# Kernel optimization log

Measured on AMD Instinct MI355X. Metric: run time of the kernel, lower is better.

Reference implementation:

```python
import jax, jax.numpy as jnp
import numpy as np

N, E = 50000, 800000
IN_DIM, HIDDEN, OUT_DIM, LAYERS = 128, 64, 40, 3


def setup_inputs() -> dict:
    key = jax.random.key(0)
    ks = jax.random.split(key, 12)
    glorot = lambda k, fi, fo: jax.random.normal(k, (fi, fo), jnp.float32) * np.sqrt(2.0 / (fi + fo)).astype(np.float32)
    return {
        "x": jax.random.normal(ks[0], (N, IN_DIM), jnp.float32),
        "edge_index": jax.random.randint(ks[1], (2, E), 0, N, jnp.int64),
        "edge_weight": jax.random.uniform(ks[2], (E,), jnp.float32),
        "W1": glorot(ks[3], IN_DIM, HIDDEN), "b1": jnp.zeros((HIDDEN,), jnp.float32),
        "W2": glorot(ks[4], HIDDEN, HIDDEN), "b2": jnp.zeros((HIDDEN,), jnp.float32),
        "W3": glorot(ks[5], HIDDEN, HIDDEN), "b3": jnp.zeros((HIDDEN,), jnp.float32),
        "Wlin": glorot(ks[6], HIDDEN * LAYERS, OUT_DIM), "blin": jnp.zeros((OUT_DIM,), jnp.float32),
    }


def reference(x, edge_index, edge_weight, W1, b1, W2, b2, W3, b3, Wlin, blin):
    src, dst = edge_index[0], edge_index[1]

    def gcn_conv(h, W, b):
        # GCNConv with normalize=False: linear transform, then weighted sum aggregation at dst, then bias.
        h = h @ W                                   # [N, hidden]
        msg = h[src] * edge_weight[:, None]          # [E, hidden] gather + scale
        agg = jax.ops.segment_sum(msg, dst, num_segments=h.shape[0])  # scatter-add
        return agg + b

    outs = []
    h = x
    for W, b in ((W1, b1), (W2, b2), (W3, b3)):
        h = jax.nn.relu(gcn_conv(h, W, b))           # dropout is identity at inference
        outs.append(h)

    hjk = jnp.concatenate(outs, axis=-1)             # JumpingKnowledge mode='cat' -> [N, hidden*layers]
    return hjk @ Wlin + blin                         # [N, out_dim]
```

## Files before the change

### kernel.cpp

```cpp
#include <hip/hip_runtime.h>

#define HID 64
#define JK_DIM 192
#define OUT_DIM 40
#define AP 136
#define HP 72
#define W_PITCH 196
#define FG_PITCH 44

typedef __attribute__((ext_vector_type(8))) short bf16x8;
typedef __attribute__((ext_vector_type(4))) float f32x4;

__device__ inline unsigned short f2b(float f) {
    unsigned u = __float_as_uint(f);
    unsigned r = u + 0x7FFF + ((u >> 16) & 1);
    return (unsigned short)(r >> 16);
}
__device__ inline float b2f(unsigned short u) {
    return __uint_as_float(((unsigned)u) << 16);
}
__device__ inline float blo(unsigned u) { return __uint_as_float(u << 16); }
__device__ inline float bhi(unsigned u) { return __uint_as_float(u & 0xFFFF0000u); }
__device__ inline unsigned pack2(float a, float b) {
    return (unsigned)f2b(a) | ((unsigned)f2b(b) << 16);
}

__global__ __launch_bounds__(256) void prep(int* __restrict__ deg, int n,
                                            const float* __restrict__ W,
                                            float* __restrict__ Wt,
                                            int* __restrict__ gctr) {
    int i = blockIdx.x * 256 + threadIdx.x;
    if (i == 0) gctr[0] = 0;
    if (i < n) deg[i] = 0;
    if (i < JK_DIM * OUT_DIM) {
        int k = i / OUT_DIM;
        int c = i - k * OUT_DIM;
        Wt[c * JK_DIM + k] = W[i];
    }
}

__global__ __launch_bounds__(256) void hist_dst(const int* __restrict__ dst,
                                                int* __restrict__ deg,
                                                unsigned short* __restrict__ rank,
                                                int E, int part) {
    int p = blockIdx.x & 7;
    int bid = blockIdx.x >> 3;
    int nblk = gridDim.x >> 3;
    int lo = p * part, hi = lo + part;
    int E4 = E >> 2;
    for (int q = bid * 256 + threadIdx.x; q < E4; q += nblk * 256) {
        int4 d4 = ((const int4*)dst)[q];
        int e = q * 4;
        if (d4.x >= lo && d4.x < hi) rank[e + 0] = (unsigned short)atomicAdd(&deg[d4.x], 1);
        if (d4.y >= lo && d4.y < hi) rank[e + 1] = (unsigned short)atomicAdd(&deg[d4.y], 1);
        if (d4.z >= lo && d4.z < hi) rank[e + 2] = (unsigned short)atomicAdd(&deg[d4.z], 1);
        if (d4.w >= lo && d4.w < hi) rank[e + 3] = (unsigned short)atomicAdd(&deg[d4.w], 1);
    }
    if (bid == 0 && threadIdx.x < (E & 3)) {
        int e = (E & ~3) + threadIdx.x;
        int d = dst[e];
        if (d >= lo && d < hi) rank[e] = (unsigned short)atomicAdd(&deg[d], 1);
    }
}

__global__ __launch_bounds__(256) void scan_fused(const int* __restrict__ deg,
                                                  int* __restrict__ off,
                                                  int* __restrict__ gctr, int n) {
    __shared__ int tmp[256];
    __shared__ int base;
    int i = blockIdx.x * 256 + threadIdx.x;
    int v = (i < n) ? deg[i] : 0;
    tmp[threadIdx.x] = v;
    __syncthreads();
    for (int d = 1; d < 256; d <<= 1) {
        int t = (threadIdx.x >= d) ? tmp[threadIdx.x - d] : 0;
        __syncthreads();
        tmp[threadIdx.x] += t;
        __syncthreads();
    }
    if (threadIdx.x == 255) base = atomicAdd(gctr, tmp[255]);
    __syncthreads();
    if (i < n) off[i] = base + tmp[threadIdx.x] - v;
}

__global__ __launch_bounds__(256) void fill_and_gemm(
        const int* __restrict__ src, const int* __restrict__ dst,
        const float* __restrict__ ew, const int* __restrict__ off,
        const unsigned short* __restrict__ rank,
        unsigned* __restrict__ ecsr, int E,
        const float* __restrict__ x, const float* __restrict__ W1,
        unsigned short* __restrict__ linb, int n, int nFill) {
    __shared__ unsigned short Ah[64 * AP];
    __shared__ unsigned short Wt[64 * AP];
    int tid = threadIdx.x;
    if ((int)blockIdx.x < nFill) {
        int q = blockIdx.x * 256 + tid;
        int E4 = E >> 2;
        if (q < E4) {
            int4 d4 = ((const int4*)dst)[q];
            int4 s4 = ((const int4*)src)[q];
            float4 wv = ((const float4*)ew)[q];
            ushort4 r4 = ((const ushort4*)rank)[q];
            ecsr[off[d4.x] + r4.x] = (unsigned)s4.x | ((unsigned)f2b(wv.x) << 16);
            ecsr[off[d4.y] + r4.y] = (unsigned)s4.y | ((unsigned)f2b(wv.y) << 16);
            ecsr[off[d4.z] + r4.z] = (unsigned)s4.z | ((unsigned)f2b(wv.z) << 16);
            ecsr[off[d4.w] + r4.w] = (unsigned)s4.w | ((unsigned)f2b(wv.w) << 16);
        }
        if (blockIdx.x == 0 && tid < (E & 3)) {
            int e = (E & ~3) + tid;
            int d = dst[e];
            ecsr[off[d] + rank[e]] = (unsigned)src[e] | ((unsigned)f2b(ew[e]) << 16);
        }
        return;
    }
    int row0 = (blockIdx.x - nFill) * 64;
    if (row0 >= n) return;
    for (int i = tid; i < 64 * 32; i += 256) {
        int r = i >> 5;
        int c4 = (i & 31) * 4;
        int grow = row0 + r;
        if (grow >= n) grow = n - 1;
        float4 v = *(const float4*)(x + (long)grow * 128 + c4);
        ushort4 o;
        o.x = f2b(v.x); o.y = f2b(v.y); o.z = f2b(v.z); o.w = f2b(v.w);
        *(ushort4*)(Ah + r * AP + c4) = o;
    }
    for (int i = tid; i < 128 * 16; i += 256) {
        int k = i >> 4;
        int n4 = (i & 15) * 4;
        float4 v = *(const float4*)(W1 + (long)k * 64 + n4);
        Wt[(n4 + 0) * AP + k] = f2b(v.x);
        Wt[(n4 + 1) * AP + k] = f2b(v.y);
        Wt[(n4 + 2) * AP + k] = f2b(v.z);
        Wt[(n4 + 3) * AP + k] = f2b(v.w);
    }
    __syncthreads();

    int wave = tid >> 6;
    int lane = tid & 63;
    int lr = lane & 15;
    int lk = (lane >> 4) * 8;
    f32x4 acc[4];
#pragma unroll
    for (int nf = 0; nf < 4; ++nf) acc[nf] = (f32x4){0.f, 0.f, 0.f, 0.f};
#pragma unroll
    for (int k0 = 0; k0 < 128; k0 += 32) {
        bf16x8 a = *(const bf16x8*)(Ah + (wave * 16 + lr) * AP + k0 + lk);
#pragma unroll
        for (int nf = 0; nf < 4; ++nf) {
            bf16x8 b = *(const bf16x8*)(Wt + (nf * 16 + lr) * AP + k0 + lk);
            acc[nf] = __builtin_amdgcn_mfma_f32_16x16x32_bf16(a, b, acc[nf], 0, 0, 0);
        }
    }
    int mbase = wave * 16 + (lane >> 4) * 4;
#pragma unroll
    for (int nf = 0; nf < 4; ++nf) {
#pragma unroll
        for (int r = 0; r < 4; ++r) {
            int grow = row0 + mbase + r;
            if (grow < n)
                linb[(long)grow * HID + nf * 16 + lr] = f2b(acc[nf][r]);
        }
    }
}

__global__ __launch_bounds__(256) void aggregate(const unsigned short* __restrict__ linb,
                                                 const unsigned* __restrict__ ecsr,
                                                 const int* __restrict__ off,
                                                 const int* __restrict__ deg,
                                                 const float* __restrict__ bias,
                                                 unsigned short* __restrict__ hout, int n) {
    int cl = threadIdx.x & 7;
    float4 bLo = *(const float4*)(bias + cl * 8);
    float4 bHi = *(const float4*)(bias + cl * 8 + 4);
    int grp = (blockIdx.x * 256 + threadIdx.x) >> 3;
    int ngrp = (gridDim.x * 256) >> 3;
    for (int node = grp; node < n; node += ngrp) {
        int start = off[node];
        int cnt = deg[node];
        float acc[8];
#pragma unroll
        for (int i = 0; i < 8; ++i) acc[i] = 0.f;

        int s[8];
        float w[8];
#pragma unroll
        for (int t = 0; t < 8; ++t) {
            s[t] = 0; w[t] = 0.f;
            if (t < cnt) {
                unsigned m = ecsr[start + t];
                s[t] = (int)(m & 0xFFFFu);
                w[t] = b2f((unsigned short)(m >> 16));
            }
        }
        for (int bb = 0; bb < cnt; bb += 8) {
            int s2[8];
            float w2[8];
#pragma unroll
            for (int t = 0; t < 8; ++t) {
                int e = bb + 8 + t;
                s2[t] = 0; w2[t] = 0.f;
                if (e < cnt) {
                    unsigned m = ecsr[start + e];
                    s2[t] = (int)(m & 0xFFFFu);
                    w2[t] = b2f((unsigned short)(m >> 16));
                }
            }
            uint4 u[8];
#pragma unroll
            for (int t = 0; t < 8; ++t)
                u[t] = *(const uint4*)(linb + (long)s[t] * HID + cl * 8);
#pragma unroll
            for (int t = 0; t < 8; ++t) {
                acc[0] += blo(u[t].x) * w[t];
                acc[1] += bhi(u[t].x) * w[t];
                acc[2] += blo(u[t].y) * w[t];
                acc[3] += bhi(u[t].y) * w[t];
                acc[4] += blo(u[t].z) * w[t];
                acc[5] += bhi(u[t].z) * w[t];
                acc[6] += blo(u[t].w) * w[t];
                acc[7] += bhi(u[t].w) * w[t];
            }
#pragma unroll
            for (int t = 0; t < 8; ++t) { s[t] = s2[t]; w[t] = w2[t]; }
        }

        uint4 o;
        o.x = pack2(fmaxf(acc[0] + bLo.x, 0.f), fmaxf(acc[1] + bLo.y, 0.f));
        o.y = pack2(fmaxf(acc[2] + bLo.z, 0.f), fmaxf(acc[3] + bLo.w, 0.f));
        o.z = pack2(fmaxf(acc[4] + bHi.x, 0.f), fmaxf(acc[5] + bHi.y, 0.f));
        o.w = pack2(fmaxf(acc[6] + bHi.z, 0.f), fmaxf(acc[7] + bHi.w, 0.f));
        *(uint4*)(hout + (long)node * JK_DIM + cl * 8) = o;
    }
}

__global__ __launch_bounds__(256) void agg_transform(
        const unsigned short* __restrict__ hprev,
        const unsigned* __restrict__ ecsr,
        const int* __restrict__ off, const int* __restrict__ deg,
        const float* __restrict__ W, const float* __restrict__ bias,
        unsigned short* __restrict__ hout, int n) {
    __shared__ unsigned short Hs[64 * HP];
    __shared__ unsigned short Wt[64 * HP];
    int tid = threadIdx.x;
    int row0 = blockIdx.x * 64;
    if (row0 >= n) return;
    for (int i = tid; i < 64 * 16; i += 256) {
        int k = i >> 4;
        int n4 = (i & 15) * 4;
        float4 v = *(const float4*)(W + (long)k * 64 + n4);
        Wt[(n4 + 0) * HP + k] = f2b(v.x);
        Wt[(n4 + 1) * HP + k] = f2b(v.y);
        Wt[(n4 + 2) * HP + k] = f2b(v.z);
        Wt[(n4 + 3) * HP + k] = f2b(v.w);
    }
    int cl = tid & 7;
    int g0 = tid >> 3;
    for (int gi = 0; gi < 2; ++gi) {
        int lrow = g0 + gi * 32;
        int node = row0 + lrow;
        float acc[8];
#pragma unroll
        for (int i = 0; i < 8; ++i) acc[i] = 0.f;
        if (node < n) {
            int start = off[node];
            int cnt = deg[node];
            int s[8];
            float w[8];
#pragma unroll
            for (int t = 0; t < 8; ++t) {
                s[t] = 0; w[t] = 0.f;
                if (t < cnt) {
                    unsigned m = ecsr[start + t];
                    s[t] = (int)(m & 0xFFFFu);
                    w[t] = b2f((unsigned short)(m >> 16));
                }
            }
            for (int bb = 0; bb < cnt; bb += 8) {
                int s2[8];
                float w2[8];
#pragma unroll
                for (int t = 0; t < 8; ++t) {
                    int e = bb + 8 + t;
                    s2[t] = 0; w2[t] = 0.f;
                    if (e < cnt) {
                        unsigned m = ecsr[start + e];
                        s2[t] = (int)(m & 0xFFFFu);
                        w2[t] = b2f((unsigned short)(m >> 16));
                    }
                }
                uint4 u[8];
#pragma unroll
                for (int t = 0; t < 8; ++t)
                    u[t] = *(const uint4*)(hprev + (long)s[t] * JK_DIM + cl * 8);
#pragma unroll
                for (int t = 0; t < 8; ++t) {
                    acc[0] += blo(u[t].x) * w[t];
                    acc[1] += bhi(u[t].x) * w[t];
                    acc[2] += blo(u[t].y) * w[t];
                    acc[3] += bhi(u[t].y) * w[t];
                    acc[4] += blo(u[t].z) * w[t];
                    acc[5] += bhi(u[t].z) * w[t];
                    acc[6] += blo(u[t].w) * w[t];
                    acc[7] += bhi(u[t].w) * w[t];
                }
#pragma unroll
                for (int t = 0; t < 8; ++t) { s[t] = s2[t]; w[t] = w2[t]; }
            }
        }
        uint4 o;
        o.x = pack2(acc[0], acc[1]);
        o.y = pack2(acc[2], acc[3]);
        o.z = pack2(acc[4], acc[5]);
        o.w = pack2(acc[6], acc[7]);
        *(uint4*)(Hs + lrow * HP + cl * 8) = o;
    }
    __syncthreads();
    int wave = tid >> 6;
    int lane = tid & 63;
    int lr = lane & 15;
    int lk = (lane >> 4) * 8;
    f32x4 d[4];
#pragma unroll
    for (int nf = 0; nf < 4; ++nf) d[nf] = (f32x4){0.f, 0.f, 0.f, 0.f};
#pragma unroll
    for (int k0 = 0; k0 < 64; k0 += 32) {
        bf16x8 a = *(const bf16x8*)(Hs + (wave * 16 + lr) * HP + k0 + lk);
#pragma unroll
        for (int nf = 0; nf < 4; ++nf) {
            bf16x8 b = *(const bf16x8*)(Wt + (nf * 16 + lr) * HP + k0 + lk);
            d[nf] = __builtin_amdgcn_mfma_f32_16x16x32_bf16(a, b, d[nf], 0, 0, 0);
        }
    }
    int mbase = wave * 16 + (lane >> 4) * 4;
#pragma unroll
    for (int nf = 0; nf < 4; ++nf) {
        float bv = bias[nf * 16 + lr];
#pragma unroll
        for (int r = 0; r < 4; ++r) {
            int grow = row0 + mbase + r;
            if (grow < n)
                hout[(long)grow * JK_DIM + nf * 16 + lr] = f2b(fmaxf(d[nf][r] + bv, 0.f));
        }
    }
}

__global__ __launch_bounds__(256) void final_gemm(const unsigned short* __restrict__ hcat,
                                                  const float* __restrict__ Wt,
                                                  const float* __restrict__ b,
                                                  float* __restrict__ out, int n) {
    __shared__ float pool[OUT_DIM * W_PITCH];
    int tid = threadIdx.x;
    for (int i = tid; i < OUT_DIM * 48; i += 256) {
        int c = i / 48;
        int q = (i - c * 48) * 4;
        *(float4*)(pool + c * W_PITCH + q) = *(const float4*)(Wt + (long)c * JK_DIM + q);
    }
    __syncthreads();

    int rg = tid >> 3;
    int cg = tid & 7;
    int c0 = cg * 5;
    int row0 = blockIdx.x * 64;
    int r0 = row0 + rg * 2;
    int ra = r0 < n ? r0 : n - 1;
    int rb = r0 + 1 < n ? r0 + 1 : n - 1;
    const unsigned short* ha = hcat + (long)ra * JK_DIM;
    const unsigned short* hb = hcat + (long)rb * JK_DIM;

    float acc[2][5];
#pragma unroll
    for (int r = 0; r < 2; ++r)
#pragma unroll
        for (int i = 0; i < 5; ++i) acc[r][i] = 0.f;

#pragma unroll 4
    for (int k = 0; k < JK_DIM; k += 4) {
        uint2 ua = *(const uint2*)(ha + k);
        uint2 ub = *(const uint2*)(hb + k);
        float4 va = make_float4(blo(ua.x), bhi(ua.x), blo(ua.y), bhi(ua.y));
        float4 vb = make_float4(blo(ub.x), bhi(ub.x), blo(ub.y), bhi(ub.y));
        float4 w0 = *(const float4*)(pool + (c0 + 0) * W_PITCH + k);
        float4 w1 = *(const float4*)(pool + (c0 + 1) * W_PITCH + k);
        float4 w2 = *(const float4*)(pool + (c0 + 2) * W_PITCH + k);
        float4 w3 = *(const float4*)(pool + (c0 + 3) * W_PITCH + k);
        float4 w4 = *(const float4*)(pool + (c0 + 4) * W_PITCH + k);
        acc[0][0] += va.x * w0.x + va.y * w0.y + va.z * w0.z + va.w * w0.w;
        acc[0][1] += va.x * w1.x + va.y * w1.y + va.z * w1.z + va.w * w1.w;
        acc[0][2] += va.x * w2.x + va.y * w2.y + va.z * w2.z + va.w * w2.w;
        acc[0][3] += va.x * w3.x + va.y * w3.y + va.z * w3.z + va.w * w3.w;
        acc[0][4] += va.x * w4.x + va.y * w4.y + va.z * w4.z + va.w * w4.w;
        acc[1][0] += vb.x * w0.x + vb.y * w0.y + vb.z * w0.z + vb.w * w0.w;
        acc[1][1] += vb.x * w1.x + vb.y * w1.y + vb.z * w1.z + vb.w * w1.w;
        acc[1][2] += vb.x * w2.x + vb.y * w2.y + vb.z * w2.z + vb.w * w2.w;
        acc[1][3] += vb.x * w3.x + vb.y * w3.y + vb.z * w3.z + vb.w * w3.w;
        acc[1][4] += vb.x * w4.x + vb.y * w4.y + vb.z * w4.z + vb.w * w4.w;
    }

    __syncthreads();
#pragma unroll
    for (int r = 0; r < 2; ++r)
#pragma unroll
        for (int i = 0; i < 5; ++i)
            pool[(rg * 2 + r) * FG_PITCH + c0 + i] = acc[r][i] + b[c0 + i];
    __syncthreads();

    if (row0 + 64 <= n) {
        for (int i = tid; i < 64 * OUT_DIM / 4; i += 256) {
            int f = i * 4;
            int row = f / OUT_DIM;
            int col = f - row * OUT_DIM;
            *(float4*)(out + (long)(row0 + row) * OUT_DIM + col) =
                *(const float4*)(pool + row * FG_PITCH + col);
        }
    } else {
        for (int i = tid; i < 64 * OUT_DIM; i += 256) {
            int row = i / OUT_DIM;
            int col = i - row * OUT_DIM;
            if (row0 + row < n)
                out[(long)(row0 + row) * OUT_DIM + col] = pool[row * FG_PITCH + col];
        }
    }
}

extern "C" void kernel_launch(void* const* d_in, const int* in_sizes, int n_in,
                              void* d_out, int out_size, void* d_ws, size_t ws_size,
                              hipStream_t stream) {
    const float* x    = (const float*)d_in[0];
    const int*   ei   = (const int*)d_in[1];
    const float* ew   = (const float*)d_in[2];
    const float* W1   = (const float*)d_in[3];
    const float* b1   = (const float*)d_in[4];
    const float* W2   = (const float*)d_in[5];
    const float* b2   = (const float*)d_in[6];
    const float* W3   = (const float*)d_in[7];
    const float* b3   = (const float*)d_in[8];
    const float* Wlin = (const float*)d_in[9];
    const float* blin = (const float*)d_in[10];
    float* out = (float*)d_out;

    const int N = in_sizes[0] / 128;
    const int E = in_sizes[2];
    const int* src = ei;
    const int* dst = ei + E;
    const int PART = (N + 7) / 8;

    char* wsb = (char*)d_ws;
    unsigned short* linb  = (unsigned short*)wsb;   wsb += (long)N * HID * 2;
    unsigned short* hcatb = (unsigned short*)wsb;   wsb += (long)N * JK_DIM * 2;
    int* deg    = (int*)wsb;                        wsb += (long)N * 4;
    int* off    = (int*)wsb;                        wsb += (long)N * 4;
    int* bsum   = (int*)wsb;                        wsb += 256 * 4;
    float* Wt   = (float*)wsb;                      wsb += (long)JK_DIM * OUT_DIM * 4;
    unsigned* ecsr = (unsigned*)wsb;
    unsigned short* rank = hcatb;
    int* gctr = bsum;

    dim3 blk(256);
    const int nblkN = (N + 255) / 256;
    dim3 gN(nblkN);
    dim3 gHist(8 * 104);
    const int nFill = ((E >> 2) + 255) / 256;
    const int nGemm = (N + 63) / 64;
    dim3 gFG(nFill + nGemm);
    dim3 gTile((N + 63) / 64);
    dim3 gAgg((N + 31) / 32);
    dim3 gFin((N + 63) / 64);

    unsigned short* h1 = hcatb;
    unsigned short* h2 = hcatb + HID;
    unsigned short* h3 = hcatb + 2 * HID;

    prep<<<gN, blk, 0, stream>>>(deg, N, Wlin, Wt, gctr);
    hist_dst<<<gHist, blk, 0, stream>>>(dst, deg, rank, E, PART);
    scan_fused<<<gN, blk, 0, stream>>>(deg, off, gctr, N);

    fill_and_gemm<<<gFG, blk, 0, stream>>>(src, dst, ew, off, rank, ecsr, E,
                                           x, W1, linb, N, nFill);
    aggregate<<<gAgg, blk, 0, stream>>>(linb, ecsr, off, deg, b1, h1, N);

    agg_transform<<<gTile, blk, 0, stream>>>(h1, ecsr, off, deg, W2, b2, h2, N);
    agg_transform<<<gTile, blk, 0, stream>>>(h2, ecsr, off, deg, W3, b3, h3, N);

    final_gemm<<<gFin, blk, 0, stream>>>(hcatb, Wt, blin, out, N);
}
```

Measured before the change: 257.5 us.

## Fuse final JK linear into last agg_transform and balance rows via atomic counter

Removes the separate final_gemm kernel by computing the JumpingKnowledge output projection inside the third-layer agg_transform. The layer-3 activations stay in shared memory instead of being written to and re-read from global memory, and the Wlin weights are read from global/L1 rather than staged in LDS. It also replaces the fixed two-rows-per-group split of the aggregation loop with a shared atomic row counter, so groups of 8 lanes pull rows dynamically to even out uneven degree work. The fused tail does more per-thread scalar FMAs with uncoalesced weight loads and raises register pressure.

```diff
diff --git a/kernel.cpp b/kernel.cpp
--- a/kernel.cpp
+++ b/kernel.cpp
@@ -5,8 +5,6 @@
 #define OUT_DIM 40
 #define AP 136
 #define HP 72
-#define W_PITCH 196
-#define FG_PITCH 44
 
 typedef __attribute__((ext_vector_type(8))) short bf16x8;
 typedef __attribute__((ext_vector_type(4))) float f32x4;
@@ -239,12 +237,18 @@
         const unsigned* __restrict__ ecsr,
         const int* __restrict__ off, const int* __restrict__ deg,
         const float* __restrict__ W, const float* __restrict__ bias,
-        unsigned short* __restrict__ hout, int n) {
+        unsigned short* __restrict__ hout, int n,
+        const unsigned short* __restrict__ hcat,
+        const float* __restrict__ WtLin,
+        const float* __restrict__ blin,
+        float* __restrict__ outp) {
     __shared__ unsigned short Hs[64 * HP];
     __shared__ unsigned short Wt[64 * HP];
+    __shared__ int nextRow;
     int tid = threadIdx.x;
     int row0 = blockIdx.x * 64;
     if (row0 >= n) return;
+    if (tid == 0) nextRow = 0;
     for (int i = tid; i < 64 * 16; i += 256) {
         int k = i >> 4;
         int n4 = (i & 15) * 4;
@@ -254,10 +258,14 @@
         Wt[(n4 + 2) * HP + k] = f2b(v.z);
         Wt[(n4 + 3) * HP + k] = f2b(v.w);
     }
+    __syncthreads();
     int cl = tid & 7;
-    int g0 = tid >> 3;
-    for (int gi = 0; gi < 2; ++gi) {
-        int lrow = g0 + gi * 32;
+    int laneBase = (tid & 63) & ~7;
+    for (;;) {
+        int lrow;
+        if ((tid & 7) == 0) lrow = atomicAdd(&nextRow, 1);
+        lrow = __shfl(lrow, laneBase, 64);
+        if (lrow >= 64) break;
         int node = row0 + lrow;
         float acc[8];
 #pragma unroll
@@ -333,94 +341,71 @@
         }
     }
     int mbase = wave * 16 + (lane >> 4) * 4;
+    if (!WtLin) {
+#pragma unroll
+        for (int nf = 0; nf < 4; ++nf) {
+            float bv = bias[nf * 16 + lr];
+#pragma unroll
+            for (int r = 0; r < 4; ++r) {
+                int grow = row0 + mbase + r;
+                if (grow < n)
+                    hout[(long)grow * JK_DIM + nf * 16 + lr] = f2b(fmaxf(d[nf][r] + bv, 0.f));
+            }
+        }
+        return;
+    }
+    __syncthreads();
+    unsigned short* H3s = Wt;
 #pragma unroll
     for (int nf = 0; nf < 4; ++nf) {
         float bv = bias[nf * 16 + lr];
 #pragma unroll
-        for (int r = 0; r < 4; ++r) {
-            int grow = row0 + mbase + r;
-            if (grow < n)
-                hout[(long)grow * JK_DIM + nf * 16 + lr] = f2b(fmaxf(d[nf][r] + bv, 0.f));
-        }
-    }
-}
-
-__global__ __launch_bounds__(256) void final_gemm(const unsigned short* __restrict__ hcat,
-                                                  const float* __restrict__ Wt,
-                                                  const float* __restrict__ b,
-                                                  float* __restrict__ out, int n) {
-    __shared__ float pool[OUT_DIM * W_PITCH];
-    int tid = threadIdx.x;
-    for (int i = tid; i < OUT_DIM * 48; i += 256) {
-        int c = i / 48;
-        int q = (i - c * 48) * 4;
-        *(float4*)(pool + c * W_PITCH + q) = *(const float4*)(Wt + (long)c * JK_DIM + q);
-    }
-    __syncthreads();
-
-    int rg = tid >> 3;
-    int cg = tid & 7;
-    int c0 = cg * 5;
-    int row0 = blockIdx.x * 64;
-    int r0 = row0 + rg * 2;
-    int ra = r0 < n ? r0 : n - 1;
-    int rb = r0 + 1 < n ? r0 + 1 : n - 1;
-    const unsigned short* ha = hcat + (long)ra * JK_DIM;
-    const unsigned short* hb = hcat + (long)rb * JK_DIM;
-
-    float acc[2][5];
-#pragma unroll
-    for (int r = 0; r < 2; ++r)
-#pragma unroll
-        for (int i = 0; i < 5; ++i) acc[r][i] = 0.f;
-
-#pragma unroll 4
-    for (int k = 0; k < JK_DIM; k += 4) {
-        uint2 ua = *(const uint2*)(ha + k);
-        uint2 ub = *(const uint2*)(hb + k);
-        float4 va = make_float4(blo(ua.x), bhi(ua.x), blo(ua.y), bhi(ua.y));
-        float4 vb = make_float4(blo(ub.x), bhi(ub.x), blo(ub.y), bhi(ub.y));
-        float4 w0 = *(const float4*)(pool + (c0 + 0) * W_PITCH + k);
-        float4 w1 = *(const float4*)(pool + (c0 + 1) * W_PITCH + k);
-        float4 w2 = *(const float4*)(pool + (c0 + 2) * W_PITCH + k);
-        float4 w3 = *(const float4*)(pool + (c0 + 3) * W_PITCH + k);
-        float4 w4 = *(const float4*)(pool + (c0 + 4) * W_PITCH + k);
-        acc[0][0] += va.x * w0.x + va.y * w0.y + va.z * w0.z + va.w * w0.w;
-        acc[0][1] += va.x * w1.x + va.y * w1.y + va.z * w1.z + va.w * w1.w;
-        acc[0][2] += va.x * w2.x + va.y * w2.y + va.z * w2.z + va.w * w2.w;
-        acc[0][3] += va.x * w3.x + va.y * w3.y + va.z * w3.z + va.w * w3.w;
-        acc[0][4] += va.x * w4.x + va.y * w4.y + va.z * w4.z + va.w * w4.w;
-        acc[1][0] += vb.x * w0.x + vb.y * w0.y + vb.z * w0.z + vb.w * w0.w;
-        acc[1][1] += vb.x * w1.x + vb.y * w1.y + vb.z * w1.z + vb.w * w1.w;
-        acc[1][2] += vb.x * w2.x + vb.y * w2.y + vb.z * w2.z + vb.w * w2.w;
-        acc[1][3] += vb.x * w3.x + vb.y * w3.y + vb.z * w3.z + vb.w * w3.w;
-        acc[1][4] += vb.x * w4.x + vb.y * w4.y + vb.z * w4.z + vb.w * w4.w;
-    }
-
-    __syncthreads();
-#pragma unroll
-    for (int r = 0; r < 2; ++r)
-#pragma unroll
-        for (int i = 0; i < 5; ++i)
-            pool[(rg * 2 + r) * FG_PITCH + c0 + i] = acc[r][i] + b[c0 + i];
-    __syncthreads();
-
-    if (row0 + 64 <= n) {
-        for (int i = tid; i < 64 * OUT_DIM / 4; i += 256) {
-            int f = i * 4;
-            int row = f / OUT_DIM;
-            int col = f - row * OUT_DIM;
-            *(float4*)(out + (long)(row0 + row) * OUT_DIM + col) =
-                *(const float4*)(pool + row * FG_PITCH + col);
-        }
-    } else {
-        for (int i = tid; i < 64 * OUT_DIM; i += 256) {
-            int row = i / OUT_DIM;
-            int col = i - row * OUT_DIM;
-            if (row0 + row < n)
-                out[(long)(row0 + row) * OUT_DIM + col] = pool[row * FG_PITCH + col];
-        }
-    }
+        for (int r = 0; r < 4; ++r)
+            H3s[(mbase + r) * HP + nf * 16 + lr] = f2b(fmaxf(d[nf][r] + bv, 0.f));
+    }
+    __syncthreads();
+    int r = tid >> 2;
+    int cg = tid & 3;
+    int c0 = cg * 10;
+    int node = row0 + r;
+    if (node >= n) return;
+    float acc2[10];
+#pragma unroll
+    for (int i = 0; i < 10; ++i) acc2[i] = 0.f;
+    const unsigned short* hrow = hcat + (long)node * JK_DIM;
+#pragma unroll
+    for (int b8 = 0; b8 < 16; ++b8) {
+        uint4 u = *(const uint4*)(hrow + b8 * 8);
+        float h[8];
+        h[0] = blo(u.x); h[1] = bhi(u.x);
+        h[2] = blo(u.y); h[3] = bhi(u.y);
+        h[4] = blo(u.z); h[5] = bhi(u.z);
+        h[6] = blo(u.w); h[7] = bhi(u.w);
+#pragma unroll
+        for (int half = 0; half < 2; ++half) {
+            int k0 = b8 * 8 + half * 4;
+#pragma unroll
+            for (int i = 0; i < 10; ++i) {
+                float4 wv = *(const float4*)(WtLin + (long)(c0 + i) * JK_DIM + k0);
+                acc2[i] += h[half * 4 + 0] * wv.x + h[half * 4 + 1] * wv.y
+                         + h[half * 4 + 2] * wv.z + h[half * 4 + 3] * wv.w;
+            }
+        }
+    }
+#pragma unroll
+    for (int b4 = 0; b4 < 16; ++b4) {
+        uint2 p = *(const uint2*)(H3s + r * HP + b4 * 4);
+        float h0 = blo(p.x), h1v = bhi(p.x), h2v = blo(p.y), h3v = bhi(p.y);
+        int k0 = 128 + b4 * 4;
+#pragma unroll
+        for (int i = 0; i < 10; ++i) {
+            float4 wv = *(const float4*)(WtLin + (long)(c0 + i) * JK_DIM + k0);
+            acc2[i] += h0 * wv.x + h1v * wv.y + h2v * wv.z + h3v * wv.w;
+        }
+    }
+#pragma unroll
+    for (int i = 0; i < 10; ++i)
+        outp[(long)node * OUT_DIM + c0 + i] = acc2[i] + blin[c0 + i];
 }
 
 extern "C" void kernel_launch(void* const* d_in, const int* in_sizes, int n_in,
@@ -465,7 +450,6 @@
     dim3 gFG(nFill + nGemm);
     dim3 gTile((N + 63) / 64);
     dim3 gAgg((N + 31) / 32);
-    dim3 gFin((N + 63) / 64);
 
     unsigned short* h1 = hcatb;
     unsigned short* h2 = hcatb + HID;
@@ -479,8 +463,9 @@
                                            x, W1, linb, N, nFill);
     aggregate<<<gAgg, blk, 0, stream>>>(linb, ecsr, off, deg, b1, h1, N);
 
-    agg_transform<<<gTile, blk, 0, stream>>>(h1, ecsr, off, deg, W2, b2, h2, N);
-    agg_transform<<<gTile, blk, 0, stream>>>(h2, ecsr, off, deg, W3, b3, h3, N);
-
-    final_gemm<<<gFin, blk, 0, stream>>>(hcatb, Wt, blin, out, N);
-}
+    agg_transform<<<gTile, blk, 0, stream>>>(h1, ecsr, off, deg, W2, b2, h2, N,
+                                             nullptr, nullptr, nullptr, nullptr);
+    agg_transform<<<gTile, blk, 0, stream>>>(h2, ecsr, off, deg, W3, b3, h3, N,
+                                             hcatb, Wt, blin, out);
+    (void)h3;
+}
```

After: 497.5 us. 93.2% more time.
